# Optimization experiments

Hardware: AMD Instinct MI355X
Metric: run time of the kernel (lower is better)

The kernel has to match this reference:

```python
import jax, jax.numpy as jnp
import numpy as np

B, R, C = 2, 64, 256
PH = PW = 7
KMAX = 8            # max pool-kernel size per axis given roi size bounds (kernel<=7 here)
HW = [160, 80, 40, 20]   # FPN level spatial sizes for a 640px image, strides 4/8/16/32
STRIDES = [4.0, 8.0, 16.0, 32.0]
TOP = 224.0         # config.top_pyramid_roi_size
HIDDEN = 2048
NCLS = 20
SCALE = float(np.round(np.sqrt(C), 2))  # np.round(sqrt(inner_dim),2) in SelfAttention


def setup_inputs() -> dict:
    key = jax.random.key(0)
    ks = jax.random.split(key, 32)
    U = lambda k, s, lo, hi: jax.random.uniform(k, s, minval=lo, maxval=hi)
    x1 = U(ks[0], (B, R), 0.0, 260.0)
    y1 = U(ks[1], (B, R), 0.0, 260.0)
    w = U(ks[2], (B, R), 16.0, 360.0)
    h = U(ks[3], (B, R), 16.0, 360.0)
    rois = jnp.stack([x1, y1, jnp.minimum(x1 + w, 639.0), jnp.minimum(y1 + h, 639.0)], -1)
    N = lambda k, s, sc: (sc * jax.random.normal(k, s)).astype(jnp.float32)
    inp = {'rois': rois}
    for i in range(4):
        inp[f'fm{i}'] = N(ks[4 + i], (B, C, HW[i], HW[i]), 1.0)
    inp['wq'] = N(ks[8], (C, C), 0.02);  inp['bq'] = jnp.zeros((C,), jnp.float32)
    inp['wk'] = N(ks[9], (C, C), 0.02);  inp['bk'] = jnp.zeros((C,), jnp.float32)
    inp['wv'] = N(ks[10], (C, C), 0.02); inp['bv'] = jnp.zeros((C,), jnp.float32)
    inp['wo'] = N(ks[11], (C, C), 0.02); inp['bo'] = jnp.zeros((C,), jnp.float32)
    inp['w1'] = N(ks[12], (C * PH * PW, HIDDEN), 0.02); inp['b1'] = jnp.zeros((HIDDEN,), jnp.float32)
    inp['w2'] = N(ks[13], (HIDDEN, HIDDEN), 0.02);       inp['b2'] = jnp.zeros((HIDDEN,), jnp.float32)
    inp['wreg'] = N(ks[14], (HIDDEN, 4 * (NCLS + 1)), 0.02); inp['breg'] = jnp.zeros((4 * (NCLS + 1),), jnp.float32)
    inp['wcls'] = N(ks[15], (HIDDEN, NCLS + 1), 0.02);       inp['bcls'] = jnp.zeros((NCLS + 1,), jnp.float32)
    return inp


def _forward(rois, fm0, fm1, fm2, fm3, wq, bq, wk, bk, wv, bv, wo, bo,
             w1, b1, w2, b2, wreg, breg, wcls, bcls):
    Hmax = HW[0]
    pad = lambda fm: jnp.pad(fm, ((0, 0), (0, 0), (0, Hmax - fm.shape[-2]), (0, Hmax - fm.shape[-1])))
    feats = jnp.stack([pad(fm0), pad(fm1), pad(fm2), pad(fm3)])  # [4,B,C,Hmax,Hmax]
    heights = jnp.array(HW, jnp.int32)
    strides = jnp.array(STRIDES, jnp.float32)

    r = rois.reshape(-1, 4)                 # [N,4] xyxy in pixels
    Nroi = r.shape[0]
    bidx = jnp.repeat(jnp.arange(B, dtype=jnp.int32), R)
    size = jnp.sqrt((r[:, 2] - r[:, 0]) * (r[:, 3] - r[:, 1]))
    # int() truncates toward zero, then clamp(0,3) -- matches torch
    lvl = jnp.clip((3.0 + jnp.log(size / TOP)).astype(jnp.int32), 0, 3)
    s = strides[lvl]
    x1 = (r[:, 0] / s).astype(jnp.int32); y1 = (r[:, 1] / s).astype(jnp.int32)
    x2 = (r[:, 2] / s).astype(jnp.int32); y2 = (r[:, 3] / s).astype(jnp.int32)
    Hl = heights[lvl]                        # per-roi level map size (square maps)

    def expand(lo, hi, cap, pool):
        # replicate the symmetric while-loop expansion until span >= pool
        for _ in range(pool):
            need = (hi - lo + 1) < pool
            lo = jnp.where(need, jnp.maximum(lo - 1, 0), lo)
            hi = jnp.where(need, jnp.minimum(hi + 1, cap - 1), hi)
        return lo, hi

    y1, y2 = expand(y1, y2, Hl, PH)
    x1, x2 = expand(x1, x2, Hl, PW)
    rh = y2 - y1 + 1; rw = x2 - x1 + 1
    kh = (rh + PH - 1) // PH; sh = rh // PH   # ceil / floor kernel & stride
    kw = (rw + PW - 1) // PW; sw = rw // PW

    ar_p = jnp.arange(PH); ar_k = jnp.arange(KMAX)

    def pool_one(l, b, yy, xx, kh_, kw_, sh_, sw_):
        rows = jnp.clip(yy + ar_p[:, None] * sh_ + ar_k[None, :], 0, Hmax - 1)  # [PH,K]
        cols = jnp.clip(xx + ar_p[:, None] * sw_ + ar_k[None, :], 0, Hmax - 1)  # [PW,K]
        patch = feats[l, b][:, rows[:, :, None, None], cols[None, None, :, :]]  # [C,PH,K,PW,K]
        m = (ar_k < kh_)[:, None, None] & (ar_k < kw_)[None, None, :]           # [K,1,K] -> bcast
        patch = jnp.where(m, patch, -jnp.inf)
        return patch.max(axis=(2, 4))                                           # [C,PH,PW]

    pooled = jax.vmap(pool_one)(lvl, bidx, y1, x1, kh, kw, sh, sw)  # [N,C,PH,PW]

    # SelfAttention over the PH*PW spatial tokens of each ROI
    L = PH * PW
    tok = pooled.reshape(Nroi, C, L).transpose(0, 2, 1)            # [N,L,C]
    q = tok @ wq + bq
    k = tok @ wk + bk
    v = tok @ wv + bv
    att = jax.nn.softmax(jnp.einsum('nlc,nmc->nlm', q, k) / SCALE, axis=-1)
    ctx = jnp.einsum('nlm,nmc->nlc', att, v) @ wo + bo             # [N,L,C]
    x = pooled.reshape(Nroi, C, L) + ctx.transpose(0, 2, 1)        # residual add
    x = x.reshape(Nroi, C * L)

    h1 = jax.nn.relu(x @ w1 + b1)
    h2 = jax.nn.relu(h1 @ w2 + b2)
    bbox_reg = h2 @ wreg + breg                                    # [N, 4*(NCLS+1)]
    bbox_classes = jax.nn.softmax(h2 @ wcls + bcls, axis=-1)       # [N, NCLS+1]
    return bbox_reg, bbox_classes


def reference(rois, fm0, fm1, fm2, fm3, wq, bq, wk, bk, wv, bv, wo, bo,
              w1, b1, w2, b2, wreg, breg, wcls, bcls):
    return _forward(rois, fm0, fm1, fm2, fm3, wq, bq, wk, bk, wv, bv, wo, bo,
                    w1, b1, w2, b2, wreg, breg, wcls, bcls)
```

## Files before the change

kernel.cpp:

```cpp
#include <hip/hip_runtime.h>
#include <hip/hip_bf16.h>
#include <stdint.h>

typedef __attribute__((ext_vector_type(8))) short bf16x8;
typedef __attribute__((ext_vector_type(4))) float f32x4;

__device__ __forceinline__ float blo(unsigned u){ union{float f;unsigned x;}v; v.x = u<<16; return v.f; }
__device__ __forceinline__ float bhi(unsigned u){ union{float f;unsigned x;}v; v.x = u & 0xFFFF0000u; return v.f; }
__device__ __forceinline__ unsigned short f2bf(float f){
  union{float f;unsigned x;}v; v.f=f; unsigned x=v.x;
  return (unsigned short)((x + 0x7fffu + ((x>>16)&1u)) >> 16);
}
__device__ __forceinline__ unsigned cvtpk(float lo, float hi){
  unsigned r;
  asm("v_cvt_pk_bf16_f32 %0, %1, %2" : "=v"(r) : "v"(lo), "v"(hi));
  return r;
}

__global__ __launch_bounds__(256) void pool_pack_kernel(
    const float* __restrict__ rois,
    const float* __restrict__ fm0, const float* __restrict__ fm1,
    const float* __restrict__ fm2, const float* __restrict__ fm3,
    float* __restrict__ pooled, unsigned short* __restrict__ tok,
    const float* __restrict__ wreg, const float* __restrict__ wcls, float* __restrict__ wT,
    float* __restrict__ accz)
{
  int bx = blockIdx.x;
  int tid = threadIdx.x;
  if (bx >= 1001){
    int z = bx - 1001;
    float4 zero = {0.f,0.f,0.f,0.f};
    for (int i = z*256 + tid; i < 131072; i += 64*256) ((float4*)accz)[i] = zero;
    return;
  }
  if (bx >= 896){
    int c = bx - 896;
    if (c < 84){
      for (int k = tid; k < 2048; k += 256) wT[(size_t)c*2048 + k] = wreg[(size_t)k*84 + c];
    } else {
      int cc = c - 84;
      for (int k = tid; k < 2048; k += 256) wT[(size_t)c*2048 + k] = wcls[(size_t)k*21 + cc];
    }
    return;
  }
  int n = bx / 7;
  int ph = bx - n*7;
  int c = tid;
  const float* r = rois + n*4;
  int b = n >> 6;
  float rx1=r[0], ry1=r[1], rx2=r[2], ry2=r[3];
  float size = sqrtf((rx2-rx1)*(ry2-ry1));
  int lvl = (int)(3.0f + logf(size/224.0f));
  if (lvl < 0) lvl = 0; if (lvl > 3) lvl = 3;
  const float strides_[4] = {4.f,8.f,16.f,32.f};
  const int hw_[4] = {160,80,40,20};
  float s = strides_[lvl]; int Hl = hw_[lvl];
  int x1 = (int)(rx1/s), y1 = (int)(ry1/s), x2 = (int)(rx2/s), y2 = (int)(ry2/s);
  #pragma unroll
  for (int it=0; it<7; ++it){
    bool need = (y2-y1+1) < 7;
    if (need){ y1 = (y1-1 > 0) ? y1-1 : 0; y2 = (y2+1 < Hl-1) ? y2+1 : Hl-1; }
  }
  #pragma unroll
  for (int it=0; it<7; ++it){
    bool need = (x2-x1+1) < 7;
    if (need){ x1 = (x1-1 > 0) ? x1-1 : 0; x2 = (x2+1 < Hl-1) ? x2+1 : Hl-1; }
  }
  int rh = y2-y1+1, rw = x2-x1+1;
  int kh = (rh+6)/7, sh = rh/7, kw = (rw+6)/7, sw = rw/7;
  const float* fm = (lvl==0)?fm0:(lvl==1)?fm1:(lvl==2)?fm2:fm3;
  const float* fp = fm + ((size_t)(b*256 + c))*(size_t)(Hl*Hl);
  int r0 = y1 + ph*sh;
  for (int pw=0; pw<7; ++pw){
    int c0 = x1 + pw*sw;
    float m = -3.4e38f;
    for (int i=0;i<kh;++i){
      const float* rp = fp + (size_t)(r0+i)*Hl + c0;
      for (int j=0;j<kw;++j) m = fmaxf(m, rp[j]);
    }
    int l = ph*7+pw;
    pooled[((size_t)n*256 + c)*49 + l] = m;
    tok[((size_t)n*49 + l)*256 + c] = f2bf(m);
  }
}

template<int EPI, int ASRC>
__global__ __launch_bounds__(256) void gemm_kernel(
    const unsigned short* __restrict__ A, const float* __restrict__ Af,
    const float* __restrict__ biasA,
    const float* __restrict__ B0, const float* __restrict__ B1, const float* __restrict__ B2,
    const float* __restrict__ bias0, const float* __restrict__ bias1, const float* __restrict__ bias2,
    unsigned short* __restrict__ o0, unsigned short* __restrict__ o1, unsigned short* __restrict__ o2,
    float* __restrict__ outf, const float* __restrict__ pooled,
    int M, int Nper, int K, int nM, int nN, int kChunk)
{
  __shared__ __align__(16) unsigned short Bs[2][2048];
  int per = nM*nN;
  int kc  = blockIdx.x / per;
  int rem = blockIdx.x - kc*per;
  int bm = rem % nM, bn = rem / nM;
  int m0 = bm*64, n0 = bn*64;
  int mat = n0 / Nper;
  int col0 = n0 - mat*Nper;
  const float* Bp    = (mat==0)?B0:(mat==1)?B1:B2;
  const float* biasp = (mat==0)?bias0:(mat==1)?bias1:bias2;
  unsigned short* outp = (mat==0)?o0:(mat==1)?o1:o2;
  int k0 = kc*kChunk;
  int nMacro = kChunk >> 7;
  int tid = threadIdx.x, lane = tid & 63, wave = tid >> 6;
  int wm = wave & 1, wn = wave >> 1;
  int g = lane >> 4, c = lane & 15;

  f32x4 acc[2][2];
  #pragma unroll
  for (int i=0;i<2;++i)
    #pragma unroll
    for (int j=0;j<2;++j){ acc[i][j][0]=0.f; acc[i][j][1]=0.f; acc[i][j][2]=0.f; acc[i][j][3]=0.f; }

  int brow = tid >> 3, bcg = tid & 7;
  int bw_idx = brow*64 + ((bcg*8) ^ ((brow>>3)<<4));
  const float* Bbase = Bp + (size_t)brow*Nper + col0 + bcg*8;
  int rb0 = g*512 + (((wn*2  )^g)*16 + c);
  int rb1 = g*512 + (((wn*2+1)^g)*16 + c);
  const unsigned short* Ap0 = nullptr; const unsigned short* Ap1 = nullptr;
  const float* Hp0 = nullptr; const float* Hp1 = nullptr; const float* Bip = nullptr;
  if constexpr (ASRC==0){
    Ap0 = A + (size_t)(m0 + wm*32 +      c)*K + g*8;
    Ap1 = A + (size_t)(m0 + wm*32 + 16 + c)*K + g*8;
  } else {
    Hp0 = Af + (size_t)(m0 + wm*32 +      c)*K + g*8;
    Hp1 = Af + (size_t)(m0 + wm*32 + 16 + c)*K + g*8;
    Bip = biasA + g*8;
  }

  auto writeB = [&](int buf, const float4& bx, const float4& by){
    uint4 w;
    w.x = cvtpk(bx.x,bx.y); w.y = cvtpk(bx.z,bx.w);
    w.z = cvtpk(by.x,by.y); w.w = cvtpk(by.z,by.w);
    *(uint4*)&Bs[buf][bw_idx] = w;
  };
  auto readFrags = [&](int buf, bf16x8& r0, bf16x8& r1){
    union { unsigned short s[8]; bf16x8 v; } u0, u1;
    const unsigned short* bsp = &Bs[buf][0];
    #pragma unroll
    for (int j=0;j<8;++j){ u0.s[j] = bsp[rb0 + j*64]; u1.s[j] = bsp[rb1 + j*64]; }
    r0 = u0.v; r1 = u1.v;
  };
  auto makeA1 = [&](int kk, bf16x8& fa0, bf16x8& fa1){
    float4 x0 = *(const float4*)(Hp0+kk), x1 = *(const float4*)(Hp0+kk+4);
    float4 y0 = *(const float4*)(Hp1+kk), y1 = *(const float4*)(Hp1+kk+4);
    float4 c0 = *(const float4*)(Bip+kk), c1 = *(const float4*)(Bip+kk+4);
    union { unsigned u[4]; bf16x8 v; } t0, t1;
    t0.u[0] = cvtpk(fmaxf(x0.x+c0.x,0.f), fmaxf(x0.y+c0.y,0.f));
    t0.u[1] = cvtpk(fmaxf(x0.z+c0.z,0.f), fmaxf(x0.w+c0.w,0.f));
    t0.u[2] = cvtpk(fmaxf(x1.x+c1.x,0.f), fmaxf(x1.y+c1.y,0.f));
    t0.u[3] = cvtpk(fmaxf(x1.z+c1.z,0.f), fmaxf(x1.w+c1.w,0.f));
    t1.u[0] = cvtpk(fmaxf(y0.x+c0.x,0.f), fmaxf(y0.y+c0.y,0.f));
    t1.u[1] = cvtpk(fmaxf(y0.z+c0.z,0.f), fmaxf(y0.w+c0.w,0.f));
    t1.u[2] = cvtpk(fmaxf(y1.x+c1.x,0.f), fmaxf(y1.y+c1.y,0.f));
    t1.u[3] = cvtpk(fmaxf(y1.z+c1.z,0.f), fmaxf(y1.w+c1.w,0.f));
    fa0 = t0.v; fa1 = t1.v;
  };
  auto mfma4 = [&](const bf16x8& f0, const bf16x8& f1, const bf16x8& q0, const bf16x8& q1){
    acc[0][0] = __builtin_amdgcn_mfma_f32_16x16x32_bf16(f0,q0,acc[0][0],0,0,0);
    acc[0][1] = __builtin_amdgcn_mfma_f32_16x16x32_bf16(f0,q1,acc[0][1],0,0,0);
    acc[1][0] = __builtin_amdgcn_mfma_f32_16x16x32_bf16(f1,q0,acc[1][0],0,0,0);
    acc[1][1] = __builtin_amdgcn_mfma_f32_16x16x32_bf16(f1,q1,acc[1][1],0,0,0);
  };

  for (int mi = 0; mi < nMacro; ++mi){
    int kk = k0 + (mi << 7);
    uint4 a0x,a0y,a1x,a1y,a2x,a2y,a3x,a3y;
    if constexpr (ASRC==0){
      a0x = *(const uint4*)(Ap0+kk);    a0y = *(const uint4*)(Ap1+kk);
      a1x = *(const uint4*)(Ap0+kk+32); a1y = *(const uint4*)(Ap1+kk+32);
      a2x = *(const uint4*)(Ap0+kk+64); a2y = *(const uint4*)(Ap1+kk+64);
      a3x = *(const uint4*)(Ap0+kk+96); a3y = *(const uint4*)(Ap1+kk+96);
    }
    const float* p0 = Bbase + (size_t)kk*Nper;
    const float* p1 = p0 + (size_t)32*Nper;
    const float* p2 = p0 + (size_t)64*Nper;
    const float* p3 = p0 + (size_t)96*Nper;
    float4 b0a = *(const float4*)p0, b0b = *(const float4*)(p0+4);
    float4 b1a = *(const float4*)p1, b1b = *(const float4*)(p1+4);
    float4 b2a = *(const float4*)p2, b2b = *(const float4*)(p2+4);
    float4 b3a = *(const float4*)p3, b3b = *(const float4*)(p3+4);

    writeB(0, b0a, b0b);
    __syncthreads();

    bf16x8 q0,q1,f0,f1;
    readFrags(0,q0,q1);
    writeB(1,b1a,b1b);
    if constexpr (ASRC==0){ f0 = *(const bf16x8*)&a0x; f1 = *(const bf16x8*)&a0y; }
    else makeA1(kk, f0, f1);
    mfma4(f0,f1,q0,q1);
    __syncthreads();
    readFrags(1,q0,q1);
    writeB(0,b2a,b2b);
    if constexpr (ASRC==0){ f0 = *(const bf16x8*)&a1x; f1 = *(const bf16x8*)&a1y; }
    else makeA1(kk+32, f0, f1);
    mfma4(f0,f1,q0,q1);
    __syncthreads();
    readFrags(0,q0,q1);
    writeB(1,b3a,b3b);
    if constexpr (ASRC==0){ f0 = *(const bf16x8*)&a2x; f1 = *(const bf16x8*)&a2y; }
    else makeA1(kk+64, f0, f1);
    mfma4(f0,f1,q0,q1);
    __syncthreads();
    readFrags(1,q0,q1);
    if constexpr (ASRC==0){ f0 = *(const bf16x8*)&a3x; f1 = *(const bf16x8*)&a3y; }
    else makeA1(kk+96, f0, f1);
    mfma4(f0,f1,q0,q1);
  }

  int rq = g << 2, cl = c;
  #pragma unroll
  for (int mr=0;mr<2;++mr){
    #pragma unroll
    for (int nc=0;nc<2;++nc){
      int rowb = m0 + wm*32 + mr*16 + rq;
      int colM = col0 + wn*32 + nc*16 + cl;
      #pragma unroll
      for (int r2=0;r2<4;++r2){
        float v = acc[mr][nc][r2];
        int rr = rowb + r2;
        if constexpr (EPI==0){
          v += biasp[colM];
          outp[(size_t)rr*Nper + colM] = f2bf(v);
        } else if constexpr (EPI==1){
          v += biasp[colM];
          int nn = rr/49, l = rr - nn*49;
          v += pooled[((size_t)nn*256 + colM)*49 + l];
          outp[(size_t)nn*12544 + colM*49 + l] = f2bf(v);
        } else {
          atomicAdd(&outf[(size_t)rr*Nper + colM], v);
        }
      }
    }
  }
}

__global__ __launch_bounds__(256) void attn_kernel(
    const unsigned short* __restrict__ Q, const unsigned short* __restrict__ Km,
    const unsigned short* __restrict__ V, unsigned short* __restrict__ ctx)
{
  int n = blockIdx.x, half = blockIdx.y, tid = threadIdx.x;
  int r0 = half*25, rcnt = half ? 24 : 25;
  __shared__ __align__(16) unsigned short qs[25*256];
  __shared__ __align__(16) unsigned short ks[49*260];
  __shared__ float S[25*49];
  const uint4* qg = (const uint4*)(Q + ((size_t)n*49 + r0)*256);
  for (int i = tid; i < rcnt*32; i += 256) ((uint4*)qs)[i] = qg[i];
  const uint2* kg = (const uint2*)(Km + (size_t)n*49*256);
  for (int i = tid; i < 49*64; i += 256){
    int j = i >> 6, s = i & 63;
    *(uint2*)(ks + j*260 + s*4) = kg[i];
  }
  __syncthreads();
  for (int p = tid; p < rcnt*49; p += 256){
    int i = p/49, j = p - i*49;
    const uint2* qr = (const uint2*)(qs + i*256);
    const uint2* kr = (const uint2*)(ks + j*260);
    float sum = 0.f;
    #pragma unroll 8
    for (int c4 = 0; c4 < 64; ++c4){
      uint2 qv = qr[c4], kv = kr[c4];
      sum += blo(qv.x)*blo(kv.x) + bhi(qv.x)*bhi(kv.x);
      sum += blo(qv.y)*blo(kv.y) + bhi(qv.y)*bhi(kv.y);
    }
    S[p] = sum * (1.0f/16.0f);
  }
  __syncthreads();
  const uint2* vg = (const uint2*)(V + (size_t)n*49*256);
  for (int i = tid; i < 49*64; i += 256){
    int j = i >> 6, s = i & 63;
    *(uint2*)(ks + j*260 + s*4) = vg[i];
  }
  if (tid < rcnt){
    float* row = S + tid*49;
    float mx = row[0];
    for (int j=1;j<49;++j) mx = fmaxf(mx,row[j]);
    float sm = 0.f;
    for (int j=0;j<49;++j){ float e = expf(row[j]-mx); row[j]=e; sm+=e; }
    float inv = 1.0f/sm;
    for (int j=0;j<49;++j) row[j] *= inv;
  }
  __syncthreads();
  for (int idx = tid; idx < rcnt*64; idx += 256){
    int i = idx >> 6, cp4 = idx & 63;
    const float* att = S + i*49;
    float s0=0.f, s1=0.f, s2=0.f, s3=0.f;
    #pragma unroll 7
    for (int j=0;j<49;++j){
      uint2 v = *(const uint2*)(ks + j*260 + cp4*4);
      float a = att[j];
      s0 += a*blo(v.x); s1 += a*bhi(v.x);
      s2 += a*blo(v.y); s3 += a*bhi(v.y);
    }
    uint2 outw;
    outw.x = (unsigned)f2bf(s0) | ((unsigned)f2bf(s1) << 16);
    outw.y = (unsigned)f2bf(s2) | ((unsigned)f2bf(s3) << 16);
    *(uint2*)&ctx[((size_t)n*49 + r0 + i)*256 + cp4*4] = outw;
  }
}

__global__ __launch_bounds__(256) void heads_dot(
    const float* __restrict__ h2acc, const float* __restrict__ b2,
    const float* __restrict__ wT,
    const float* __restrict__ breg, const float* __restrict__ bcls,
    float* __restrict__ out, float* __restrict__ logits)
{
  int gw = (blockIdx.x*256 + threadIdx.x) >> 6;
  int lane = threadIdx.x & 63;
  int m = gw / 105, c = gw - m*105;
  const float4* hp = (const float4*)(h2acc + (size_t)m*2048);
  const float4* bp = (const float4*)b2;
  const float4* wp = (const float4*)(wT + (size_t)c*2048);
  float sum = 0.f;
  #pragma unroll
  for (int i=0;i<8;++i){
    float4 a = hp[i*64 + lane];
    float4 bb = bp[i*64 + lane];
    float4 w = wp[i*64 + lane];
    sum += fmaxf(a.x+bb.x,0.f)*w.x + fmaxf(a.y+bb.y,0.f)*w.y
         + fmaxf(a.z+bb.z,0.f)*w.z + fmaxf(a.w+bb.w,0.f)*w.w;
  }
  #pragma unroll
  for (int off=32; off; off>>=1) sum += __shfl_down(sum, off, 64);
  if (lane == 0){
    if (c < 84) out[(size_t)m*84 + c] = sum + breg[c];
    else        logits[(size_t)m*21 + (c-84)] = sum + bcls[c-84];
  }
}

__global__ __launch_bounds__(128) void cls_softmax(
    const float* __restrict__ logits, float* __restrict__ out)
{
  int m = threadIdx.x;
  const float* lg = logits + (size_t)m*21;
  float mx = lg[0];
  #pragma unroll
  for (int j=1;j<21;++j) mx = fmaxf(mx, lg[j]);
  float sm = 0.f;
  float e[21];
  #pragma unroll
  for (int j=0;j<21;++j){ e[j] = expf(lg[j]-mx); sm += e[j]; }
  float inv = 1.0f/sm;
  #pragma unroll
  for (int j=0;j<21;++j) out[10752 + (size_t)m*21 + j] = e[j]*inv;
}

extern "C" void kernel_launch(void* const* d_in, const int* in_sizes, int n_in,
                              void* d_out, int out_size, void* d_ws, size_t ws_size,
                              hipStream_t stream)
{
  (void)in_sizes; (void)n_in; (void)out_size; (void)ws_size;
  const float* rois = (const float*)d_in[0];
  const float* fm0  = (const float*)d_in[1];
  const float* fm1  = (const float*)d_in[2];
  const float* fm2  = (const float*)d_in[3];
  const float* fm3  = (const float*)d_in[4];
  const float* wq   = (const float*)d_in[5];
  const float* bq   = (const float*)d_in[6];
  const float* wk   = (const float*)d_in[7];
  const float* bk   = (const float*)d_in[8];
  const float* wv   = (const float*)d_in[9];
  const float* bv   = (const float*)d_in[10];
  const float* wo   = (const float*)d_in[11];
  const float* bo   = (const float*)d_in[12];
  const float* w1   = (const float*)d_in[13];
  const float* b1   = (const float*)d_in[14];
  const float* w2   = (const float*)d_in[15];
  const float* b2   = (const float*)d_in[16];
  const float* wreg = (const float*)d_in[17];
  const float* breg = (const float*)d_in[18];
  const float* wcls = (const float*)d_in[19];
  const float* bcls = (const float*)d_in[20];
  float* out = (float*)d_out;

  char* ws = (char*)d_ws;
  float*          pooled = (float*)(ws + 0);
  unsigned short* tok    = (unsigned short*)(ws + 6422528);
  unsigned short* Qb     = (unsigned short*)(ws + 9633792);
  unsigned short* Kb     = (unsigned short*)(ws + 12845056);
  unsigned short* Vb     = (unsigned short*)(ws + 16056320);
  unsigned short* ctx    = (unsigned short*)(ws + 19267584);
  unsigned short* xb     = (unsigned short*)(ws + 22478848);
  float*          h1acc  = (float*)(ws + 25690112);
  float*          h2acc  = (float*)(ws + 26738688);
  float*          wT     = (float*)(ws + 27787264);
  float*          logits = (float*)(ws + 28647424);

  pool_pack_kernel<<<1065,256,0,stream>>>(rois, fm0, fm1, fm2, fm3, pooled, tok,
                                          wreg, wcls, wT, h1acc);

  gemm_kernel<0,0><<<1176,256,0,stream>>>(tok, nullptr, nullptr, wq,wk,wv, bq,bk,bv,
                                          Qb,Kb,Vb, nullptr, nullptr, 6272,256,256, 98,12, 256);

  attn_kernel<<<dim3(128,2),256,0,stream>>>(Qb, Kb, Vb, ctx);

  gemm_kernel<1,0><<<392,256,0,stream>>>(ctx, nullptr, nullptr, wo,wo,wo, bo,bo,bo,
                                         xb,xb,xb, nullptr, pooled, 6272,256,256, 98,4, 256);

  gemm_kernel<2,0><<<896,256,0,stream>>>(xb, nullptr, nullptr, w1,w1,w1,
                                         nullptr,nullptr,nullptr, nullptr,nullptr,nullptr,
                                         h1acc, nullptr, 128,2048,12544, 2,32, 896);

  gemm_kernel<2,1><<<1024,256,0,stream>>>(nullptr, h1acc, b1, w2,w2,w2,
                                          nullptr,nullptr,nullptr, nullptr,nullptr,nullptr,
                                          h2acc, nullptr, 128,2048,2048, 2,32, 128);

  heads_dot<<<3360,256,0,stream>>>(h2acc, b2, wT, breg, bcls, out, logits);
  cls_softmax<<<1,128,0,stream>>>(logits, out);
}
```

Measured before the change: 191.5 us.

## Replace atomic split-K accumulation with partial buffers and reduce kernels

The split-K GEMMs for the two hidden layers now write per-chunk partial results to a scratch buffer instead of using atomicAdd into a zeroed accumulator. Two new reduction kernels sum the partials: the first adds bias, applies ReLU and converts to bf16 so the second GEMM can read bf16 A directly, and the second writes fp32 h2. This drops the zeroing blocks from the pool kernel and the fp32-to-bf16 A conversion path in the GEMM. The cost is extra global traffic for the partial buffers and two additional launches, and the partials reuse the pooled region of the workspace.

```diff
diff --git a/kernel.cpp b/kernel.cpp
--- a/kernel.cpp
+++ b/kernel.cpp
@@ -22,17 +22,10 @@
     const float* __restrict__ fm0, const float* __restrict__ fm1,
     const float* __restrict__ fm2, const float* __restrict__ fm3,
     float* __restrict__ pooled, unsigned short* __restrict__ tok,
-    const float* __restrict__ wreg, const float* __restrict__ wcls, float* __restrict__ wT,
-    float* __restrict__ accz)
+    const float* __restrict__ wreg, const float* __restrict__ wcls, float* __restrict__ wT)
 {
   int bx = blockIdx.x;
   int tid = threadIdx.x;
-  if (bx >= 1001){
-    int z = bx - 1001;
-    float4 zero = {0.f,0.f,0.f,0.f};
-    for (int i = z*256 + tid; i < 131072; i += 64*256) ((float4*)accz)[i] = zero;
-    return;
-  }
   if (bx >= 896){
     int c = bx - 896;
     if (c < 84){
@@ -84,10 +77,9 @@
   }
 }
 
-template<int EPI, int ASRC>
+template<int EPI>
 __global__ __launch_bounds__(256) void gemm_kernel(
-    const unsigned short* __restrict__ A, const float* __restrict__ Af,
-    const float* __restrict__ biasA,
+    const unsigned short* __restrict__ A,
     const float* __restrict__ B0, const float* __restrict__ B1, const float* __restrict__ B2,
     const float* __restrict__ bias0, const float* __restrict__ bias1, const float* __restrict__ bias2,
     unsigned short* __restrict__ o0, unsigned short* __restrict__ o1, unsigned short* __restrict__ o2,
@@ -122,16 +114,8 @@
   const float* Bbase = Bp + (size_t)brow*Nper + col0 + bcg*8;
   int rb0 = g*512 + (((wn*2  )^g)*16 + c);
   int rb1 = g*512 + (((wn*2+1)^g)*16 + c);
-  const unsigned short* Ap0 = nullptr; const unsigned short* Ap1 = nullptr;
-  const float* Hp0 = nullptr; const float* Hp1 = nullptr; const float* Bip = nullptr;
-  if constexpr (ASRC==0){
-    Ap0 = A + (size_t)(m0 + wm*32 +      c)*K + g*8;
-    Ap1 = A + (size_t)(m0 + wm*32 + 16 + c)*K + g*8;
-  } else {
-    Hp0 = Af + (size_t)(m0 + wm*32 +      c)*K + g*8;
-    Hp1 = Af + (size_t)(m0 + wm*32 + 16 + c)*K + g*8;
-    Bip = biasA + g*8;
-  }
+  const unsigned short* Ap0 = A + (size_t)(m0 + wm*32 +      c)*K + g*8;
+  const unsigned short* Ap1 = A + (size_t)(m0 + wm*32 + 16 + c)*K + g*8;
 
   auto writeB = [&](int buf, const float4& bx, const float4& by){
     uint4 w;
@@ -146,21 +130,6 @@
     for (int j=0;j<8;++j){ u0.s[j] = bsp[rb0 + j*64]; u1.s[j] = bsp[rb1 + j*64]; }
     r0 = u0.v; r1 = u1.v;
   };
-  auto makeA1 = [&](int kk, bf16x8& fa0, bf16x8& fa1){
-    float4 x0 = *(const float4*)(Hp0+kk), x1 = *(const float4*)(Hp0+kk+4);
-    float4 y0 = *(const float4*)(Hp1+kk), y1 = *(const float4*)(Hp1+kk+4);
-    float4 c0 = *(const float4*)(Bip+kk), c1 = *(const float4*)(Bip+kk+4);
-    union { unsigned u[4]; bf16x8 v; } t0, t1;
-    t0.u[0] = cvtpk(fmaxf(x0.x+c0.x,0.f), fmaxf(x0.y+c0.y,0.f));
-    t0.u[1] = cvtpk(fmaxf(x0.z+c0.z,0.f), fmaxf(x0.w+c0.w,0.f));
-    t0.u[2] = cvtpk(fmaxf(x1.x+c1.x,0.f), fmaxf(x1.y+c1.y,0.f));
-    t0.u[3] = cvtpk(fmaxf(x1.z+c1.z,0.f), fmaxf(x1.w+c1.w,0.f));
-    t1.u[0] = cvtpk(fmaxf(y0.x+c0.x,0.f), fmaxf(y0.y+c0.y,0.f));
-    t1.u[1] = cvtpk(fmaxf(y0.z+c0.z,0.f), fmaxf(y0.w+c0.w,0.f));
-    t1.u[2] = cvtpk(fmaxf(y1.x+c1.x,0.f), fmaxf(y1.y+c1.y,0.f));
-    t1.u[3] = cvtpk(fmaxf(y1.z+c1.z,0.f), fmaxf(y1.w+c1.w,0.f));
-    fa0 = t0.v; fa1 = t1.v;
-  };
   auto mfma4 = [&](const bf16x8& f0, const bf16x8& f1, const bf16x8& q0, const bf16x8& q1){
     acc[0][0] = __builtin_amdgcn_mfma_f32_16x16x32_bf16(f0,q0,acc[0][0],0,0,0);
     acc[0][1] = __builtin_amdgcn_mfma_f32_16x16x32_bf16(f0,q1,acc[0][1],0,0,0);
@@ -170,13 +139,10 @@
 
   for (int mi = 0; mi < nMacro; ++mi){
     int kk = k0 + (mi << 7);
-    uint4 a0x,a0y,a1x,a1y,a2x,a2y,a3x,a3y;
-    if constexpr (ASRC==0){
-      a0x = *(const uint4*)(Ap0+kk);    a0y = *(const uint4*)(Ap1+kk);
-      a1x = *(const uint4*)(Ap0+kk+32); a1y = *(const uint4*)(Ap1+kk+32);
-      a2x = *(const uint4*)(Ap0+kk+64); a2y = *(const uint4*)(Ap1+kk+64);
-      a3x = *(const uint4*)(Ap0+kk+96); a3y = *(const uint4*)(Ap1+kk+96);
-    }
+    uint4 a0x = *(const uint4*)(Ap0+kk),    a0y = *(const uint4*)(Ap1+kk);
+    uint4 a1x = *(const uint4*)(Ap0+kk+32), a1y = *(const uint4*)(Ap1+kk+32);
+    uint4 a2x = *(const uint4*)(Ap0+kk+64), a2y = *(const uint4*)(Ap1+kk+64);
+    uint4 a3x = *(const uint4*)(Ap0+kk+96), a3y = *(const uint4*)(Ap1+kk+96);
     const float* p0 = Bbase + (size_t)kk*Nper;
     const float* p1 = p0 + (size_t)32*Nper;
     const float* p2 = p0 + (size_t)64*Nper;
@@ -189,29 +155,24 @@
     writeB(0, b0a, b0b);
     __syncthreads();
 
-    bf16x8 q0,q1,f0,f1;
+    bf16x8 q0,q1;
     readFrags(0,q0,q1);
     writeB(1,b1a,b1b);
-    if constexpr (ASRC==0){ f0 = *(const bf16x8*)&a0x; f1 = *(const bf16x8*)&a0y; }
-    else makeA1(kk, f0, f1);
-    mfma4(f0,f1,q0,q1);
+    mfma4(*(const bf16x8*)&a0x, *(const bf16x8*)&a0y, q0,q1);
     __syncthreads();
+
     readFrags(1,q0,q1);
     writeB(0,b2a,b2b);
-    if constexpr (ASRC==0){ f0 = *(const bf16x8*)&a1x; f1 = *(const bf16x8*)&a1y; }
-    else makeA1(kk+32, f0, f1);
-    mfma4(f0,f1,q0,q1);
+    mfma4(*(const bf16x8*)&a1x, *(const bf16x8*)&a1y, q0,q1);
     __syncthreads();
+
     readFrags(0,q0,q1);
     writeB(1,b3a,b3b);
-    if constexpr (ASRC==0){ f0 = *(const bf16x8*)&a2x; f1 = *(const bf16x8*)&a2y; }
-    else makeA1(kk+64, f0, f1);
-    mfma4(f0,f1,q0,q1);
+    mfma4(*(const bf16x8*)&a2x, *(const bf16x8*)&a2y, q0,q1);
     __syncthreads();
+
     readFrags(1,q0,q1);
-    if constexpr (ASRC==0){ f0 = *(const bf16x8*)&a3x; f1 = *(const bf16x8*)&a3y; }
-    else makeA1(kk+96, f0, f1);
-    mfma4(f0,f1,q0,q1);
+    mfma4(*(const bf16x8*)&a3x, *(const bf16x8*)&a3y, q0,q1);
   }
 
   int rq = g << 2, cl = c;
@@ -234,11 +195,41 @@
           v += pooled[((size_t)nn*256 + colM)*49 + l];
           outp[(size_t)nn*12544 + colM*49 + l] = f2bf(v);
         } else {
-          atomicAdd(&outf[(size_t)rr*Nper + colM], v);
+          outf[(size_t)kc*M*Nper + (size_t)rr*Nper + colM] = v;
         }
       }
     }
   }
+}
+
+__global__ __launch_bounds__(256) void reduce1_kernel(
+    const float* __restrict__ part, const float* __restrict__ b1,
+    unsigned short* __restrict__ h1, int nPart)
+{
+  int i = blockIdx.x*256 + threadIdx.x;
+  float4 s = ((const float4*)part)[i];
+  for (int kc = 1; kc < nPart; ++kc){
+    float4 p = ((const float4*)part)[(size_t)kc*65536 + i];
+    s.x += p.x; s.y += p.y; s.z += p.z; s.w += p.w;
+  }
+  float4 bb = *(const float4*)(b1 + ((i<<2) & 2047));
+  s.x = fmaxf(s.x+bb.x,0.f); s.y = fmaxf(s.y+bb.y,0.f);
+  s.z = fmaxf(s.z+bb.z,0.f); s.w = fmaxf(s.w+bb.w,0.f);
+  uint2 w;
+  w.x = cvtpk(s.x, s.y); w.y = cvtpk(s.z, s.w);
+  *(uint2*)&h1[(size_t)i<<2] = w;
+}
+
+__global__ __launch_bounds__(256) void reduce2_kernel(
+    const float* __restrict__ part, float* __restrict__ h2f, int nPart)
+{
+  int i = blockIdx.x*256 + threadIdx.x;
+  float4 s = ((const float4*)part)[i];
+  for (int kc = 1; kc < nPart; ++kc){
+    float4 p = ((const float4*)part)[(size_t)kc*65536 + i];
+    s.x += p.x; s.y += p.y; s.z += p.z; s.w += p.w;
+  }
+  ((float4*)h2f)[i] = s;
 }
 
 __global__ __launch_bounds__(256) void attn_kernel(
@@ -306,7 +297,7 @@
 }
 
 __global__ __launch_bounds__(256) void heads_dot(
-    const float* __restrict__ h2acc, const float* __restrict__ b2,
+    const float* __restrict__ h2f, const float* __restrict__ b2,
     const float* __restrict__ wT,
     const float* __restrict__ breg, const float* __restrict__ bcls,
     float* __restrict__ out, float* __restrict__ logits)
@@ -314,7 +305,7 @@
   int gw = (blockIdx.x*256 + threadIdx.x) >> 6;
   int lane = threadIdx.x & 63;
   int m = gw / 105, c = gw - m*105;
-  const float4* hp = (const float4*)(h2acc + (size_t)m*2048);
+  const float4* hp = (const float4*)(h2f + (size_t)m*2048);
   const float4* bp = (const float4*)b2;
   const float4* wp = (const float4*)(wT + (size_t)c*2048);
   float sum = 0.f;
@@ -387,30 +378,34 @@
   unsigned short* Vb     = (unsigned short*)(ws + 16056320);
   unsigned short* ctx    = (unsigned short*)(ws + 19267584);
   unsigned short* xb     = (unsigned short*)(ws + 22478848);
-  float*          h1acc  = (float*)(ws + 25690112);
-  float*          h2acc  = (float*)(ws + 26738688);
+  float*          h2f    = (float*)(ws + 25690112);
+  unsigned short* h1     = (unsigned short*)(ws + 26738688);
   float*          wT     = (float*)(ws + 27787264);
   float*          logits = (float*)(ws + 28647424);
-
-  pool_pack_kernel<<<1065,256,0,stream>>>(rois, fm0, fm1, fm2, fm3, pooled, tok,
-                                          wreg, wcls, wT, h1acc);
-
-  gemm_kernel<0,0><<<1176,256,0,stream>>>(tok, nullptr, nullptr, wq,wk,wv, bq,bk,bv,
-                                          Qb,Kb,Vb, nullptr, nullptr, 6272,256,256, 98,12, 256);
+  float*          h1part = (float*)(ws + 0);
+  float*          h2part = (float*)(ws + 0);
+
+  pool_pack_kernel<<<1001,256,0,stream>>>(rois, fm0, fm1, fm2, fm3, pooled, tok,
+                                          wreg, wcls, wT);
+
+  gemm_kernel<0><<<1176,256,0,stream>>>(tok, wq,wk,wv, bq,bk,bv,
+                                        Qb,Kb,Vb, nullptr, nullptr, 6272,256,256, 98,12, 256);
 
   attn_kernel<<<dim3(128,2),256,0,stream>>>(Qb, Kb, Vb, ctx);
 
-  gemm_kernel<1,0><<<392,256,0,stream>>>(ctx, nullptr, nullptr, wo,wo,wo, bo,bo,bo,
-                                         xb,xb,xb, nullptr, pooled, 6272,256,256, 98,4, 256);
-
-  gemm_kernel<2,0><<<896,256,0,stream>>>(xb, nullptr, nullptr, w1,w1,w1,
-                                         nullptr,nullptr,nullptr, nullptr,nullptr,nullptr,
-                                         h1acc, nullptr, 128,2048,12544, 2,32, 896);
-
-  gemm_kernel<2,1><<<1024,256,0,stream>>>(nullptr, h1acc, b1, w2,w2,w2,
-                                          nullptr,nullptr,nullptr, nullptr,nullptr,nullptr,
-                                          h2acc, nullptr, 128,2048,2048, 2,32, 128);
-
-  heads_dot<<<3360,256,0,stream>>>(h2acc, b2, wT, breg, bcls, out, logits);
+  gemm_kernel<1><<<392,256,0,stream>>>(ctx, wo,wo,wo, bo,bo,bo,
+                                       xb,xb,xb, nullptr, pooled, 6272,256,256, 98,4, 256);
+
+  gemm_kernel<2><<<896,256,0,stream>>>(xb, w1,w1,w1, nullptr,nullptr,nullptr,
+                                       nullptr,nullptr,nullptr, h1part, nullptr,
+                                       128,2048,12544, 2,32, 896);
+  reduce1_kernel<<<256,256,0,stream>>>(h1part, b1, h1, 14);
+
+  gemm_kernel<2><<<1024,256,0,stream>>>(h1, w2,w2,w2, nullptr,nullptr,nullptr,
+                                        nullptr,nullptr,nullptr, h2part, nullptr,
+                                        128,2048,2048, 2,32, 128);
+  reduce2_kernel<<<256,256,0,stream>>>(h2part, h2f, 16);
+
+  heads_dot<<<3360,256,0,stream>>>(h2f, b2, wT, breg, bcls, out, logits);
   cls_softmax<<<1,128,0,stream>>>(logits, out);
 }
```

New measurement: 189.2 us. No clear change (-1.2%).
